# Optimization experiments

Measured on AMD Instinct MI355X. Metric: run time of the kernel, lower is better.

## Reference

```python
import jax, jax.numpy as jnp
import numpy as np

EMBED = 1024
HEADS = 16
HEAD_DIM = EMBED // HEADS


def setup_inputs() -> dict:
    key = jax.random.key(0)
    ks = jax.random.split(key, 9)
    s = 1.0 / np.sqrt(EMBED)
    x = jax.random.normal(ks[0], (2, 2048, EMBED), dtype=jnp.float32)
    Wq = jax.random.uniform(ks[1], (EMBED, EMBED), jnp.float32, -s, s)
    bq = jax.random.uniform(ks[2], (EMBED,), jnp.float32, -s, s)
    Wk = jax.random.uniform(ks[3], (EMBED, EMBED), jnp.float32, -s, s)
    bk = jax.random.uniform(ks[4], (EMBED,), jnp.float32, -s, s)
    Wv = jax.random.uniform(ks[5], (EMBED, EMBED), jnp.float32, -s, s)
    bv = jax.random.uniform(ks[6], (EMBED,), jnp.float32, -s, s)
    Wo = jax.random.uniform(ks[7], (EMBED, EMBED), jnp.float32, -s, s)
    bo = jax.random.uniform(ks[8], (EMBED,), jnp.float32, -s, s)
    return {"x": x, "Wq": Wq, "bq": bq, "Wk": Wk, "bk": bk,
            "Wv": Wv, "bv": bv, "Wo": Wo, "bo": bo}


def reference(x, Wq, bq, Wk, bk, Wv, bv, Wo, bo):
    B, S, E = x.shape
    H, D = HEADS, HEAD_DIM
    # QKV projections, split heads: [B,S,E] -> [B,H,S,D]
    def proj(W, b):
        return (x @ W + b).reshape(B, S, H, D).transpose(0, 2, 1, 3)
    q, k, v = proj(Wq, bq), proj(Wk, bk), proj(Wv, bv)
    scores = jnp.einsum('bhsd,bhtd->bhst', q, k) / jnp.sqrt(jnp.float32(D))
    attn = jax.nn.softmax(scores, axis=-1)
    out = jnp.einsum('bhst,bhtd->bhsd', attn, v)  # [B,H,S,D]
    out = out.transpose(0, 2, 1, 3).reshape(B, S, E)
    return out @ Wo + bo
```

## Files before the change

### kernel.cpp

```cpp
#include <hip/hip_runtime.h>
#include <cstddef>
#include <cstdint>

#define EMB 1024
#define NH 16
#define HD 64
#define SEQ 2048
#define BATCH 2
#define MROWS 4096
#define LOG2E 1.4426950408889634f

typedef unsigned short u16;
typedef __attribute__((ext_vector_type(8))) short short8;
typedef __attribute__((ext_vector_type(4))) float floatx4;
typedef __attribute__((ext_vector_type(16))) float floatx16;
typedef __attribute__((ext_vector_type(2))) float f32x2;

#define MFMA32(a,b,c) __builtin_amdgcn_mfma_f32_16x16x32_bf16((a),(b),(c),0,0,0)
#define MFMA3216(a,b,c) __builtin_amdgcn_mfma_f32_32x32x16_bf16((a),(b),(c),0,0,0)

__device__ __forceinline__ u16 f2bf(float f) {
    union { float f; uint32_t u; } v; v.f = f;
    return (u16)((v.u + 0x7fffu + ((v.u >> 16) & 1u)) >> 16);
}
__device__ __forceinline__ uint32_t pk2u(uint32_t a, uint32_t b) {
    return __builtin_amdgcn_perm(b, a, 0x07060302u);
}
__device__ __forceinline__ float lo_f(uint32_t u) {
    union { uint32_t u; float f; } v; v.u = u << 16; return v.f;
}
__device__ __forceinline__ float hi_f(uint32_t u) {
    union { uint32_t u; float f; } v; v.u = u & 0xffff0000u; return v.f;
}
__device__ __forceinline__ void plswap(uint32_t &a, uint32_t &b) {
    asm volatile("v_permlane32_swap_b32 %0, %1" : "+v"(a), "+v"(b));
}
typedef const __attribute__((address_space(1))) void* gptr_t;
typedef __attribute__((address_space(3))) void* lptr_t;
__device__ __forceinline__ void gl2lds16(const void* g, void* l) {
    __builtin_amdgcn_global_load_lds((gptr_t)g, (lptr_t)l, 16, 0, 0);
}

__global__ __launch_bounds__(256) void cvt_all_k(
    const float* __restrict__ x,
    const float* __restrict__ W0, const float* __restrict__ W1,
    const float* __restrict__ W2, const float* __restrict__ W3,
    u16* __restrict__ Wt4, u16* __restrict__ xh) {
    const int z = blockIdx.z;
    const int tid = threadIdx.x;
    if (z == 4) {
        const int nb = gridDim.x * gridDim.y;
        const int bid = blockIdx.y * gridDim.x + blockIdx.x;
        const int stride = nb * 256 * 8;
        for (int i = (bid * 256 + tid) * 8; i < MROWS * EMB; i += stride) {
            float4 a = *(const float4*)(x + i);
            float4 b = *(const float4*)(x + i + 4);
            alignas(16) u16 o[8] = {f2bf(a.x), f2bf(a.y), f2bf(a.z), f2bf(a.w),
                                    f2bf(b.x), f2bf(b.y), f2bf(b.z), f2bf(b.w)};
            *(uint4*)(xh + i) = *(const uint4*)o;
        }
        return;
    }
    const float* W = (z == 0) ? W0 : (z == 1) ? W1 : (z == 2) ? W2 : W3;
    const float scale = (z == 0) ? 0.125f * LOG2E : 1.0f;
    u16* dst = Wt4 + (size_t)z * 1048576;
    __shared__ float Lf[64][65];
    const int kt = blockIdx.y * 64, nt = blockIdx.x * 64;
    {
        const int r = tid >> 2, c4 = (tid & 3) * 16;
        const float* src = W + (size_t)(kt + r) * EMB + nt + c4;
        #pragma unroll
        for (int i = 0; i < 16; i += 4) {
            float4 v = *(const float4*)(src + i);
            Lf[r][c4 + i + 0] = v.x; Lf[r][c4 + i + 1] = v.y;
            Lf[r][c4 + i + 2] = v.z; Lf[r][c4 + i + 3] = v.w;
        }
    }
    __syncthreads();
    const int n = tid >> 2, k4 = (tid & 3) * 16;
    alignas(16) u16 hb[16];
    #pragma unroll
    for (int i = 0; i < 16; ++i) hb[i] = f2bf(Lf[k4 + i][n] * scale);
    const size_t o = (size_t)(nt + n) * EMB + kt + k4;
    *(uint4*)(dst + o) = *(const uint4*)hb;
    *(uint4*)(dst + o + 8) = *(const uint4*)(hb + 8);
}

__global__ __launch_bounds__(256) void gemm_qkv_k(
    const u16* __restrict__ xh, const u16* __restrict__ Wt4,
    const float* __restrict__ b0, const float* __restrict__ b1,
    const float* __restrict__ b2,
    u16* __restrict__ Q, u16* __restrict__ K, u16* __restrict__ V) {
    const int flat = blockIdx.x + 8 * blockIdx.y + 256 * blockIdx.z;
    const int xcd = flat & 7, i6 = flat >> 3;
    const int z = i6 >> 5, j = i6 & 31;
    const int cm = xcd & 3, cn = xcd >> 2;
    const int bm = (cm * 8 + (j >> 2)) * 128;
    const int bn = (cn * 4 + (j & 3)) * 128;

    const u16* Wt = Wt4 + (size_t)z * 1048576;
    const float* bias = (z == 0) ? b0 : (z == 1) ? b1 : b2;
    u16* out = (z == 0) ? Q : (z == 1) ? K : V;
    const float bscale = (z == 0) ? 0.125f * LOG2E : 1.0f;
    __shared__ alignas(16) u16 As[8192];
    __shared__ alignas(16) u16 Bs[8192];
    const int tid = threadIdx.x;
    const int lane = tid & 63, w = tid >> 6;
    const int l15 = lane & 15, quad = lane >> 4;
    const int wm = (w & 1) * 64, wn = (w >> 1) * 64;

    floatx4 acc[4][4];
    const floatx4 zf = {0.f, 0.f, 0.f, 0.f};
    #pragma unroll
    for (int mt = 0; mt < 4; ++mt)
        #pragma unroll
        for (int nt = 0; nt < 4; ++nt) acc[mt][nt] = zf;

    const u16* agj[4];
    const u16* bgj[4];
    int sls[4];
    #pragma unroll
    for (int jj = 0; jj < 4; ++jj) {
        const int s = tid + 256 * jj;
        const int r = s >> 3, c = ((s & 7) - r) & 7;
        sls[jj] = s;
        agj[jj] = xh + (size_t)(bm + r) * EMB + c * 8;
        bgj[jj] = Wt + (size_t)(bn + r) * EMB + c * 8;
    }

    for (int kt = 0; kt < EMB; kt += 64) {
        __syncthreads();
        #pragma unroll
        for (int jj = 0; jj < 4; ++jj) {
            gl2lds16(agj[jj] + kt, &As[sls[jj] * 8]);
            gl2lds16(bgj[jj] + kt, &Bs[sls[jj] * 8]);
        }
        __syncthreads();
        #pragma unroll
        for (int kk = 0; kk < 2; ++kk) {
            short8 af[4], bf[4];
            #pragma unroll
            for (int t = 0; t < 4; ++t) {
                const int ra = wm + t * 16 + l15;
                const int rb = wn + t * 16 + l15;
                const int jc = kk * 4 + quad;
                af[t] = *(const short8*)&As[ra * 64 + ((jc + ra) & 7) * 8];
                bf[t] = *(const short8*)&Bs[rb * 64 + ((jc + rb) & 7) * 8];
            }
            __builtin_amdgcn_s_setprio(1);
            #pragma unroll
            for (int mt = 0; mt < 4; ++mt)
                #pragma unroll
                for (int nt = 0; nt < 4; ++nt)
                    acc[mt][nt] = MFMA32(af[mt], bf[nt], acc[mt][nt]);
            __builtin_amdgcn_s_setprio(0);
        }
    }

    #pragma unroll
    for (int nt = 0; nt < 4; ++nt) {
        const int col = bn + wn + nt * 16 + l15;
        const float bv = bias[col] * bscale;
        #pragma unroll
        for (int mt = 0; mt < 4; ++mt) {
            const int row = bm + wm + mt * 16 + quad * 4;
            #pragma unroll
            for (int r = 0; r < 4; ++r)
                out[(size_t)(row + r) * EMB + col] = f2bf(acc[mt][nt][r] + bv);
        }
    }
}

__global__ __launch_bounds__(256) void gemm_o_k(
    const u16* __restrict__ Ag, const u16* __restrict__ Wt,
    const float* __restrict__ bias, float* __restrict__ out) {
    const int flat = blockIdx.x + 16 * blockIdx.y;
    const int xcd = flat & 7, i7 = flat >> 3;
    const int bm = (xcd * 8 + (i7 >> 4)) * 64;
    const int bn = (i7 & 15) * 64;
    __shared__ alignas(16) u16 As[2][2048];
    __shared__ alignas(16) u16 Bs[2][2048];
    const int tid = threadIdx.x;
    const int lane = tid & 63, w = tid >> 6;
    const int l15 = lane & 15, quad = lane >> 4;
    const int wm = (w & 1) * 32, wn = (w >> 1) * 32;

    floatx4 acc[2][2];
    const floatx4 zf = {0.f, 0.f, 0.f, 0.f};
    #pragma unroll
    for (int mt = 0; mt < 2; ++mt)
        #pragma unroll
        for (int nt = 0; nt < 2; ++nt) acc[mt][nt] = zf;

    const int c0 = tid;
    const int r0 = c0 >> 2, p0 = c0 & 3, cc0 = (p0 - r0 - (r0 >> 2)) & 3;
    const u16* ag0 = Ag + (size_t)(bm + r0) * EMB + cc0 * 8;
    const u16* bg0 = Wt + (size_t)(bn + r0) * EMB + cc0 * 8;

    #define OSTAGE(bf, kk) do { \
        gl2lds16(ag0 + (kk), &As[bf][c0 * 8]); \
        gl2lds16(bg0 + (kk), &Bs[bf][c0 * 8]); } while (0)

    OSTAGE(0, 0);
    __syncthreads();
    for (int kt = 0; kt < EMB; kt += 32) {
        const int cur = (kt >> 5) & 1;
        if (kt + 32 < EMB) OSTAGE(cur ^ 1, kt + 32);
        short8 af[2], bf[2];
        #pragma unroll
        for (int t = 0; t < 2; ++t) {
            const int ra = wm + t * 16 + l15;
            const int rb = wn + t * 16 + l15;
            af[t] = *(const short8*)&As[cur][ra * 32 + ((quad + ra + (ra >> 2)) & 3) * 8];
            bf[t] = *(const short8*)&Bs[cur][rb * 32 + ((quad + rb + (rb >> 2)) & 3) * 8];
        }
        __builtin_amdgcn_s_setprio(1);
        #pragma unroll
        for (int mt = 0; mt < 2; ++mt)
            #pragma unroll
            for (int nt = 0; nt < 2; ++nt)
                acc[mt][nt] = MFMA32(af[mt], bf[nt], acc[mt][nt]);
        __builtin_amdgcn_s_setprio(0);
        __syncthreads();
    }

    #pragma unroll
    for (int nt = 0; nt < 2; ++nt) {
        const int col = bn + wn + nt * 16 + l15;
        const float bv = bias[col];
        #pragma unroll
        for (int mt = 0; mt < 2; ++mt) {
            const int row = bm + wm + mt * 16 + quad * 4;
            #pragma unroll
            for (int r = 0; r < 4; ++r)
                out[(size_t)(row + r) * EMB + col] = acc[mt][nt][r] + bv;
        }
    }
}

__global__ __launch_bounds__(256) void vtrans_k(const u16* __restrict__ V,
                                                u16* __restrict__ Vt) {
    const int tt = blockIdx.x, h = blockIdx.y, b = blockIdx.z;
    __shared__ u16 Lt[64][72];
    const int tid = threadIdx.x;
    {
        const int r = tid >> 2, c4 = (tid & 3) * 16;
        const u16* src = V + (size_t)(b * SEQ + tt * 64 + r) * EMB + h * HD + c4;
        alignas(16) u16 buf[16];
        *(uint4*)buf = *(const uint4*)src;
        *(uint4*)(buf + 8) = *(const uint4*)(src + 8);
        #pragma unroll
        for (int i = 0; i < 16; ++i) Lt[c4 + i][r] = buf[i];
    }
    __syncthreads();
    const int d = tid >> 2, t4 = (tid & 3) * 16;
    u16* dst = Vt + ((size_t)((b * NH + h) * HD + d)) * SEQ + tt * 64 + t4;
    *(uint4*)dst = *(const uint4*)&Lt[d][t4];
    *(uint4*)(dst + 8) = *(const uint4*)&Lt[d][t4 + 8];
}

__global__ __launch_bounds__(256) void flash_k(
    const u16* __restrict__ Q, const u16* __restrict__ K,
    const u16* __restrict__ Vt,
    u16* __restrict__ Np0, u16* __restrict__ Np1,
    u16* __restrict__ Np2, u16* __restrict__ Np3,
    float* __restrict__ Lp) {
    const int flat = blockIdx.x + 16 * blockIdx.y + 256 * blockIdx.z;
    const int xcd = flat & 7, idx = flat >> 3;
    const int gid = xcd * 16 + (idx >> 4);
    const int qt = idx & 15;
    const int h = gid & 15, zz = gid >> 4;
    const int b = zz >> 2, sp = zz & 3;
    const int t0 = sp * (SEQ / 4);
    __shared__ alignas(16) u16 Ks[2][4096];
    __shared__ alignas(16) u16 Vs[2][4096];
    const int tid = threadIdx.x;
    const int lane = tid & 63, w = tid >> 6;
    const int l31 = lane & 31, hf = lane >> 5;

    const u16* qp = Q + (size_t)(b * SEQ + qt * 128 + w * 32 + l31) * EMB
                    + h * HD + hf * 8;
    short8 qb[4];
    #pragma unroll
    for (int c = 0; c < 4; ++c) qb[c] = *(const short8*)(qp + c * 16);

    const floatx16 z16 = {0.f, 0.f, 0.f, 0.f, 0.f, 0.f, 0.f, 0.f,
                          0.f, 0.f, 0.f, 0.f, 0.f, 0.f, 0.f, 0.f};
    floatx16 oacc[2];
    oacc[0] = z16; oacc[1] = z16;
    floatx16 lacc = z16;
    const short8 ones8 = {0x3F80, 0x3F80, 0x3F80, 0x3F80,
                          0x3F80, 0x3F80, 0x3F80, 0x3F80};

    const int s0 = tid, s1 = tid + 256;
    const int kr0 = s0 >> 3, kc0 = ((s0 & 7) - kr0) & 7;
    const int kr1 = s1 >> 3, kc1 = ((s1 & 7) - kr1) & 7;
    const u16* kg0 = K + (size_t)(b * SEQ + t0 + kr0) * EMB + h * HD + kc0 * 8;
    const u16* kg1 = K + (size_t)(b * SEQ + t0 + kr1) * EMB + h * HD + kc1 * 8;
    const u16* vg0 = Vt + ((size_t)((b * NH + h) * HD + kr0)) * SEQ + t0 + kc0 * 8;
    const u16* vg1 = Vt + ((size_t)((b * NH + h) * HD + kr1)) * SEQ + t0 + kc1 * 8;

    #define FSTAGE(bf, kk) do { \
        gl2lds16(kg0 + (size_t)(kk) * 64 * EMB, &Ks[bf][s0 * 8]); \
        gl2lds16(kg1 + (size_t)(kk) * 64 * EMB, &Ks[bf][s1 * 8]); \
        gl2lds16(vg0 + (kk) * 64, &Vs[bf][s0 * 8]); \
        gl2lds16(vg1 + (kk) * 64, &Vs[bf][s1 * 8]); } while (0)

    const int NT = SEQ / 4 / 64;
    FSTAGE(0, 0);
    __syncthreads();
    for (int kt = 0; kt < NT; ++kt) {
        const int cur = kt & 1;
        if (kt + 1 < NT) FSTAGE(cur ^ 1, kt + 1);

        short8 pa[4];
        #pragma unroll
        for (int tt = 0; tt < 2; ++tt) {
            floatx16 st = z16;
            const int r = tt * 32 + l31;
            __builtin_amdgcn_s_setprio(1);
            #pragma unroll
            for (int c = 0; c < 4; ++c) {
                const int jc = c * 2 + hf;
                const short8 ka = *(const short8*)&Ks[cur][r * 64 + ((jc + r) & 7) * 8];
                st = MFMA3216(ka, qb[c], st);
            }
            __builtin_amdgcn_s_setprio(0);
            uint32_t e[16];
            #pragma unroll
            for (int i = 0; i < 16; i += 2) {
                f32x2 v = {st[i], st[i + 1]};
                v = v * 8388608.0f + 1064992512.0f;
                e[i] = (uint32_t)(int)v.x;
                e[i + 1] = (uint32_t)(int)v.y;
            }
            #pragma unroll
            for (int c = 0; c < 2; ++c) {
                uint32_t w0 = pk2u(e[c * 8 + 0], e[c * 8 + 1]);
                uint32_t w1 = pk2u(e[c * 8 + 2], e[c * 8 + 3]);
                uint32_t w2 = pk2u(e[c * 8 + 4], e[c * 8 + 5]);
                uint32_t w3 = pk2u(e[c * 8 + 6], e[c * 8 + 7]);
                plswap(w0, w2);
                plswap(w1, w3);
                union { uint32_t uu[4]; short8 s; } pk_;
                pk_.uu[0] = w0; pk_.uu[1] = w1; pk_.uu[2] = w2; pk_.uu[3] = w3;
                pa[tt * 2 + c] = pk_.s;
            }
        }

        __builtin_amdgcn_s_setprio(1);
        #pragma unroll
        for (int dt = 0; dt < 2; ++dt) {
            const int vr = dt * 32 + l31;
            #pragma unroll
            for (int g = 0; g < 4; ++g) {
                const int jc = g * 2 + hf;
                const short8 vb = *(const short8*)&Vs[cur][vr * 64 + ((jc + vr) & 7) * 8];
                oacc[dt] = MFMA3216(pa[g], vb, oacc[dt]);
            }
        }
        #pragma unroll
        for (int g = 0; g < 4; ++g) lacc = MFMA3216(pa[g], ones8, lacc);
        __builtin_amdgcn_s_setprio(0);

        __syncthreads();
    }

    u16* np = (sp == 0) ? Np0 : (sp == 1) ? Np1 : (sp == 2) ? Np2 : Np3;
    float* lp = Lp + (size_t)sp * (MROWS * NH);

    if (l31 == 0) {
        #pragma unroll
        for (int r = 0; r < 16; ++r) {
            const int qloc = (r & 3) + 8 * (r >> 2) + 4 * hf;
            const int qrow = qt * 128 + w * 32 + qloc;
            lp[(size_t)(b * SEQ + qrow) * NH + h] = lacc[r];
        }
    }

    #pragma unroll
    for (int dt = 0; dt < 2; ++dt)
        #pragma unroll
        for (int r = 0; r < 16; ++r) {
            const int qloc = (r & 3) + 8 * (r >> 2) + 4 * hf;
            const size_t o =
                (size_t)(b * SEQ + qt * 128 + w * 32 + qloc) * EMB
                + h * HD + dt * 32 + l31;
            np[o] = f2bf(oacc[dt][r]);
        }
}

__global__ __launch_bounds__(256) void reduce_k(
    const u16* __restrict__ Np0, const u16* __restrict__ Np1,
    const u16* __restrict__ Np2, const u16* __restrict__ Np3,
    const float* __restrict__ Lp, u16* __restrict__ AO) {
    const int i = blockIdx.x * 256 + threadIdx.x;
    const int e = i * 8;
    const int row = e >> 10;
    const int hh = (e & 1023) >> 6;
    const size_t lx = (size_t)row * NH + hh;
    const float lsum = Lp[lx] + Lp[(size_t)(MROWS * NH) + lx] +
                       Lp[2 * (size_t)(MROWS * NH) + lx] +
                       Lp[3 * (size_t)(MROWS * NH) + lx];
    const float inv = 1.f / lsum;
    const uint4 n0 = *(const uint4*)(Np0 + e);
    const uint4 n1 = *(const uint4*)(Np1 + e);
    const uint4 n2 = *(const uint4*)(Np2 + e);
    const uint4 n3 = *(const uint4*)(Np3 + e);
    uint4 o;
    #define RED1(q0, q1, q2, q3) \
        ((uint32_t)f2bf((lo_f(q0) + lo_f(q1) + lo_f(q2) + lo_f(q3)) * inv) | \
         ((uint32_t)f2bf((hi_f(q0) + hi_f(q1) + hi_f(q2) + hi_f(q3)) * inv) << 16))
    o.x = RED1(n0.x, n1.x, n2.x, n3.x);
    o.y = RED1(n0.y, n1.y, n2.y, n3.y);
    o.z = RED1(n0.z, n1.z, n2.z, n3.z);
    o.w = RED1(n0.w, n1.w, n2.w, n3.w);
    *(uint4*)(AO + e) = o;
}

extern "C" void kernel_launch(void* const* d_in, const int* in_sizes, int n_in,
                              void* d_out, int out_size, void* d_ws, size_t ws_size,
                              hipStream_t stream) {
    const float* x  = (const float*)d_in[0];
    const float* Wq = (const float*)d_in[1];
    const float* bq = (const float*)d_in[2];
    const float* Wk = (const float*)d_in[3];
    const float* bk = (const float*)d_in[4];
    const float* Wv = (const float*)d_in[5];
    const float* bv = (const float*)d_in[6];
    const float* Wo = (const float*)d_in[7];
    const float* bo = (const float*)d_in[8];

    u16* ws16 = (u16*)d_ws;
    const size_t P4 = (size_t)MROWS * EMB;
    u16* xh  = ws16;
    u16* Qb  = ws16 + P4;
    u16* Kb  = ws16 + 2 * P4;
    u16* Vb  = ws16 + 3 * P4;
    u16* Vtb = ws16 + 4 * P4;
    u16* Wt4 = ws16 + 5 * P4;
    u16* N2  = ws16 + 6 * P4;
    u16* N3  = ws16 + 7 * P4;
    float* Lp = (float*)(ws16 + 8 * P4);

    cvt_all_k<<<dim3(16, 16, 5), 256, 0, stream>>>(x, Wq, Wk, Wv, Wo, Wt4, xh);
    gemm_qkv_k<<<dim3(8, 32, 3), 256, 0, stream>>>(xh, Wt4, bq, bk, bv, Qb, Kb, Vb);
    vtrans_k<<<dim3(32, 16, 2), 256, 0, stream>>>(Vb, Vtb);
    flash_k<<<dim3(16, 16, 8), 256, 0, stream>>>(Qb, Kb, Vtb, xh, Vb, N2, N3, Lp);
    reduce_k<<<2048, 256, 0, stream>>>(xh, Vb, N2, N3, Lp, Qb);
    gemm_o_k<<<dim3(16, 64, 1), 256, 0, stream>>>(Qb, Wt4 + 3 * 1048576, bo, (float*)d_out);
}
```

Measured before the change: 198.3 us.

## Fuse x bf16 conversion into QKV GEMM and widen O-GEMM K tile

Drops the separate fp32-to-bf16 pass over x. The QKV GEMM now loads fp32 x directly through registers, converts it and stores the result to LDS, while W still streams via global_load_lds. Because each x tile is reused by 24 blocks, the conversion work and the fp32 reads are repeated, but the 8 MB bf16 write-then-read round trip goes away. Separately, the output GEMM replaces its double-buffered K=32 pipeline with a single-buffered K=64 tile that uses the same swizzle as the QKV GEMM, trading overlap for fewer barriers.

Result: no change. 199.9 us (+0.8%).

```diff
diff --git a/kernel.cpp b/kernel.cpp
--- a/kernel.cpp
+++ b/kernel.cpp
@@ -42,25 +42,11 @@
 }
 
 __global__ __launch_bounds__(256) void cvt_all_k(
-    const float* __restrict__ x,
     const float* __restrict__ W0, const float* __restrict__ W1,
     const float* __restrict__ W2, const float* __restrict__ W3,
-    u16* __restrict__ Wt4, u16* __restrict__ xh) {
+    u16* __restrict__ Wt4) {
     const int z = blockIdx.z;
     const int tid = threadIdx.x;
-    if (z == 4) {
-        const int nb = gridDim.x * gridDim.y;
-        const int bid = blockIdx.y * gridDim.x + blockIdx.x;
-        const int stride = nb * 256 * 8;
-        for (int i = (bid * 256 + tid) * 8; i < MROWS * EMB; i += stride) {
-            float4 a = *(const float4*)(x + i);
-            float4 b = *(const float4*)(x + i + 4);
-            alignas(16) u16 o[8] = {f2bf(a.x), f2bf(a.y), f2bf(a.z), f2bf(a.w),
-                                    f2bf(b.x), f2bf(b.y), f2bf(b.z), f2bf(b.w)};
-            *(uint4*)(xh + i) = *(const uint4*)o;
-        }
-        return;
-    }
     const float* W = (z == 0) ? W0 : (z == 1) ? W1 : (z == 2) ? W2 : W3;
     const float scale = (z == 0) ? 0.125f * LOG2E : 1.0f;
     u16* dst = Wt4 + (size_t)z * 1048576;
@@ -87,7 +73,7 @@
 }
 
 __global__ __launch_bounds__(256) void gemm_qkv_k(
-    const u16* __restrict__ xh, const u16* __restrict__ Wt4,
+    const float* __restrict__ x, const u16* __restrict__ Wt4,
     const float* __restrict__ b0, const float* __restrict__ b1,
     const float* __restrict__ b2,
     u16* __restrict__ Q, u16* __restrict__ K, u16* __restrict__ V) {
@@ -116,7 +102,7 @@
         #pragma unroll
         for (int nt = 0; nt < 4; ++nt) acc[mt][nt] = zf;
 
-    const u16* agj[4];
+    const float* agj[4];
     const u16* bgj[4];
     int sls[4];
     #pragma unroll
@@ -124,16 +110,29 @@
         const int s = tid + 256 * jj;
         const int r = s >> 3, c = ((s & 7) - r) & 7;
         sls[jj] = s;
-        agj[jj] = xh + (size_t)(bm + r) * EMB + c * 8;
+        agj[jj] = x + (size_t)(bm + r) * EMB + c * 8;
         bgj[jj] = Wt + (size_t)(bn + r) * EMB + c * 8;
     }
 
     for (int kt = 0; kt < EMB; kt += 64) {
         __syncthreads();
         #pragma unroll
+        for (int jj = 0; jj < 4; ++jj)
+            gl2lds16(bgj[jj] + kt, &Bs[sls[jj] * 8]);
+        float4 fa[4][2];
+        #pragma unroll
         for (int jj = 0; jj < 4; ++jj) {
-            gl2lds16(agj[jj] + kt, &As[sls[jj] * 8]);
-            gl2lds16(bgj[jj] + kt, &Bs[sls[jj] * 8]);
+            fa[jj][0] = *(const float4*)(agj[jj] + kt);
+            fa[jj][1] = *(const float4*)(agj[jj] + kt + 4);
+        }
+        #pragma unroll
+        for (int jj = 0; jj < 4; ++jj) {
+            alignas(16) u16 o[8] = {
+                f2bf(fa[jj][0].x), f2bf(fa[jj][0].y),
+                f2bf(fa[jj][0].z), f2bf(fa[jj][0].w),
+                f2bf(fa[jj][1].x), f2bf(fa[jj][1].y),
+                f2bf(fa[jj][1].z), f2bf(fa[jj][1].w)};
+            *(uint4*)&As[sls[jj] * 8] = *(const uint4*)o;
         }
         __syncthreads();
         #pragma unroll
@@ -178,8 +177,8 @@
     const int xcd = flat & 7, i7 = flat >> 3;
     const int bm = (xcd * 8 + (i7 >> 4)) * 64;
     const int bn = (i7 & 15) * 64;
-    __shared__ alignas(16) u16 As[2][2048];
-    __shared__ alignas(16) u16 Bs[2][2048];
+    __shared__ alignas(16) u16 As[4096];
+    __shared__ alignas(16) u16 Bs[4096];
     const int tid = threadIdx.x;
     const int lane = tid & 63, w = tid >> 6;
     const int l15 = lane & 15, quad = lane >> 4;
@@ -192,36 +191,45 @@
         #pragma unroll
         for (int nt = 0; nt < 2; ++nt) acc[mt][nt] = zf;
 
-    const int c0 = tid;
-    const int r0 = c0 >> 2, p0 = c0 & 3, cc0 = (p0 - r0 - (r0 >> 2)) & 3;
-    const u16* ag0 = Ag + (size_t)(bm + r0) * EMB + cc0 * 8;
-    const u16* bg0 = Wt + (size_t)(bn + r0) * EMB + cc0 * 8;
-
-    #define OSTAGE(bf, kk) do { \
-        gl2lds16(ag0 + (kk), &As[bf][c0 * 8]); \
-        gl2lds16(bg0 + (kk), &Bs[bf][c0 * 8]); } while (0)
-
-    OSTAGE(0, 0);
-    __syncthreads();
-    for (int kt = 0; kt < EMB; kt += 32) {
-        const int cur = (kt >> 5) & 1;
-        if (kt + 32 < EMB) OSTAGE(cur ^ 1, kt + 32);
-        short8 af[2], bf[2];
-        #pragma unroll
-        for (int t = 0; t < 2; ++t) {
-            const int ra = wm + t * 16 + l15;
-            const int rb = wn + t * 16 + l15;
-            af[t] = *(const short8*)&As[cur][ra * 32 + ((quad + ra + (ra >> 2)) & 3) * 8];
-            bf[t] = *(const short8*)&Bs[cur][rb * 32 + ((quad + rb + (rb >> 2)) & 3) * 8];
-        }
-        __builtin_amdgcn_s_setprio(1);
-        #pragma unroll
-        for (int mt = 0; mt < 2; ++mt)
-            #pragma unroll
-            for (int nt = 0; nt < 2; ++nt)
-                acc[mt][nt] = MFMA32(af[mt], bf[nt], acc[mt][nt]);
-        __builtin_amdgcn_s_setprio(0);
+    const u16* agj[2];
+    const u16* bgj[2];
+    int sls[2];
+    #pragma unroll
+    for (int jj = 0; jj < 2; ++jj) {
+        const int s = tid + 256 * jj;
+        const int r = s >> 3, c = ((s & 7) - r) & 7;
+        sls[jj] = s;
+        agj[jj] = Ag + (size_t)(bm + r) * EMB + c * 8;
+        bgj[jj] = Wt + (size_t)(bn + r) * EMB + c * 8;
+    }
+
+    for (int kt = 0; kt < EMB; kt += 64) {
         __syncthreads();
+        #pragma unroll
+        for (int jj = 0; jj < 2; ++jj) {
+            gl2lds16(agj[jj] + kt, &As[sls[jj] * 8]);
+            gl2lds16(bgj[jj] + kt, &Bs[sls[jj] * 8]);
+        }
+        __syncthreads();
+        #pragma unroll
+        for (int kk = 0; kk < 2; ++kk) {
+            short8 af[2], bf[2];
+            #pragma unroll
+            for (int t = 0; t < 2; ++t) {
+                const int ra = wm + t * 16 + l15;
+                const int rb = wn + t * 16 + l15;
+                const int jc = kk * 4 + quad;
+                af[t] = *(const short8*)&As[ra * 64 + ((jc + ra) & 7) * 8];
+                bf[t] = *(const short8*)&Bs[rb * 64 + ((jc + rb) & 7) * 8];
+            }
+            __builtin_amdgcn_s_setprio(1);
+            #pragma unroll
+            for (int mt = 0; mt < 2; ++mt)
+                #pragma unroll
+                for (int nt = 0; nt < 2; ++nt)
+                    acc[mt][nt] = MFMA32(af[mt], bf[nt], acc[mt][nt]);
+            __builtin_amdgcn_s_setprio(0);
+        }
     }
 
     #pragma unroll
@@ -433,7 +441,7 @@
 
     u16* ws16 = (u16*)d_ws;
     const size_t P4 = (size_t)MROWS * EMB;
-    u16* xh  = ws16;
+    u16* N0  = ws16;
     u16* Qb  = ws16 + P4;
     u16* Kb  = ws16 + 2 * P4;
     u16* Vb  = ws16 + 3 * P4;
@@ -443,10 +451,10 @@
     u16* N3  = ws16 + 7 * P4;
     float* Lp = (float*)(ws16 + 8 * P4);
 
-    cvt_all_k<<<dim3(16, 16, 5), 256, 0, stream>>>(x, Wq, Wk, Wv, Wo, Wt4, xh);
-    gemm_qkv_k<<<dim3(8, 32, 3), 256, 0, stream>>>(xh, Wt4, bq, bk, bv, Qb, Kb, Vb);
+    cvt_all_k<<<dim3(16, 16, 4), 256, 0, stream>>>(Wq, Wk, Wv, Wo, Wt4);
+    gemm_qkv_k<<<dim3(8, 32, 3), 256, 0, stream>>>(x, Wt4, bq, bk, bv, Qb, Kb, Vb);
     vtrans_k<<<dim3(32, 16, 2), 256, 0, stream>>>(Vb, Vtb);
-    flash_k<<<dim3(16, 16, 8), 256, 0, stream>>>(Qb, Kb, Vtb, xh, Vb, N2, N3, Lp);
-    reduce_k<<<2048, 256, 0, stream>>>(xh, Vb, N2, N3, Lp, Qb);
+    flash_k<<<dim3(16, 16, 8), 256, 0, stream>>>(Qb, Kb, Vtb, N0, Vb, N2, N3, Lp);
+    reduce_k<<<2048, 256, 0, stream>>>(N0, Vb, N2, N3, Lp, Qb);
     gemm_o_k<<<dim3(16, 64, 1), 256, 0, stream>>>(Qb, Wt4 + 3 * 1048576, bo, (float*)d_out);
 }
```
